# Kernel tuning notes

Measured on AMD Instinct MI355X. Metric: run time of the kernel, lower is better.

Reference implementation:

```python
import jax, jax.numpy as jnp
import numpy as np

B, T, H, STEPS = 8192, 128, 128, 30
BN_EPS = 1e-5


def gru_cell(x, h, w_ih, w_hh, b_ih, b_hh):
    # PyTorch GRU gate math: gates ordered (r, z, n)
    gi = x @ w_ih.T + b_ih            # [B, 3H]
    gh = h @ w_hh.T + b_hh            # [B, 3H]
    ir, iz, inn = jnp.split(gi, 3, axis=-1)
    hr, hz, hn = jnp.split(gh, 3, axis=-1)
    r = jax.nn.sigmoid(ir + hr)
    z = jax.nn.sigmoid(iz + hz)
    n = jnp.tanh(inn + r * hn)
    return (1.0 - z) * n + z * h


def setup_inputs() -> dict:
    key = jax.random.key(0)
    ks = jax.random.split(key, 10)
    s = lambda k, shape: jax.random.normal(k, shape, jnp.float32) * 0.05
    z = lambda *shape: jnp.zeros(shape, jnp.float32)
    return {
        "past": jax.random.normal(ks[0], (B, 6, T), jnp.float32),
        "conv_w": s(ks[1], (H, 6, 3)),
        "conv_b": z(H),
        "bn_gamma": jnp.ones((1,), jnp.float32),
        "bn_beta": z(1),
        "bn_mean": z(1),
        "bn_var": jnp.ones((1,), jnp.float32),
        "enc_wih": s(ks[2], (3 * H, H)),
        "enc_whh": s(ks[3], (3 * H, H)),
        "enc_bih": z(3 * H),
        "enc_bhh": z(3 * H),
        "dec_wih": s(ks[4], (3 * H, H)),
        "dec_whh": s(ks[5], (3 * H, H)),
        "dec_bih": z(3 * H),
        "dec_bhh": z(3 * H),
        "fc1_w": s(ks[6], (256, H)),
        "fc1_b": z(256),
        "fc2_w": s(ks[7], (64, 256)),
        "fc2_b": z(64),
        "fc3_w": s(ks[8], (6, 64)),
        "fc3_b": z(6),
    }


def reference(past, conv_w, conv_b, bn_gamma, bn_beta, bn_mean, bn_var,
              enc_wih, enc_whh, enc_bih, enc_bhh,
              dec_wih, dec_whh, dec_bih, dec_bhh,
              fc1_w, fc1_b, fc2_w, fc2_b, fc3_w, fc3_b):
    b = past.shape[0]
    # Conv1d(6 -> 128, k=3, pad=1) + ReLU
    y = jax.lax.conv_general_dilated(
        past, conv_w, window_strides=(1,), padding=[(1, 1)],
        dimension_numbers=("NCH", "OIH", "NCH"))
    y = jax.nn.relu(y + conv_b[None, :, None])
    # BatchNorm2d(1) in eval mode: single-channel affine normalization over whole tensor
    y = bn_gamma[0] * (y - bn_mean[0]) * jax.lax.rsqrt(bn_var[0] + BN_EPS) + bn_beta[0]
    # encoder GRU over time: [B,128,T] -> [T,B,128]
    xs = jnp.transpose(y, (2, 0, 1))
    h0 = jnp.zeros((b, H), y.dtype)

    def enc_step(h, x):
        return gru_cell(x, h, enc_wih, enc_whh, enc_bih, enc_bhh), None

    state_past, _ = jax.lax.scan(enc_step, h0, xs)  # [B,128]

    def mlp(h):
        a = jax.nn.relu(h @ fc1_w.T + fc1_b)
        a = a @ fc2_w.T + fc2_b   # no activation between fc2 and fc3 (matches Sequential)
        return a @ fc3_w.T + fc3_b

    # decoder input is state_past at step 0, zeros afterwards
    dec_inputs = jnp.concatenate(
        [state_past[None], jnp.zeros((STEPS - 1, b, H), y.dtype)], axis=0)
    present0 = past[:, :, -1]  # [B,6]

    def dec_step(carry, x):
        h, present = carry
        h = gru_cell(x, h, dec_wih, dec_whh, dec_bih, dec_bhh)
        present = present + mlp(h)
        return (h, present), present

    _, preds = jax.lax.scan(dec_step, (jnp.zeros((b, H), y.dtype), present0), dec_inputs)
    # preds: [30,B,6] -> [B,6,30] (matches prediction.permute(0,2,1))
    return jnp.transpose(preds, (1, 2, 0))
```

## Files before the change

### kernel.cpp

```cpp
#include <hip/hip_runtime.h>

#define DI __device__ __forceinline__

typedef __attribute__((ext_vector_type(8))) short short8;
typedef __attribute__((ext_vector_type(4))) float f32x4;

constexpr int THREADS = 512;
constexpr int ROWS    = 32;
constexpr int NBLK    = 8192 / ROWS;
constexpr int PITCH   = 272;
constexpr int PITCH2  = 528;
constexpr int SPITCH  = 256;

constexpr int O_STAGE = 0;
constexpr int O_PATCH = 98304;
constexpr int O_XALL  = 108544;
constexpr int O_H     = 143360;
constexpr int HBUF    = 8704;
constexpr int O_FC3W  = 160768;
constexpr int LDS_TOTAL = 162304;
constexpr int O_A1D   = 98304;
constexpr int O_W32   = 115200;
constexpr int O_B32   = 123648;

DI unsigned cvtpk2(float lo, float hi){
  unsigned r;
  asm("v_cvt_pk_bf16_f32 %0, %1, %2" : "=v"(r) : "v"(lo), "v"(hi));
  return r;
}
DI unsigned short f2bf(float f){ return (unsigned short)cvtpk2(f, f); }
DI float u2f_lo(unsigned u){ union { unsigned u; float f; } v; v.u = u << 16;        return v.f; }
DI float u2f_hi(unsigned u){ union { unsigned u; float f; } v; v.u = u & 0xffff0000u; return v.f; }
DI float sigm(float x){ return __builtin_amdgcn_rcpf(1.f + __expf(-x)); }
DI float tanh_(float x){ return 2.f * __builtin_amdgcn_rcpf(1.f + __expf(-2.f * x)) - 1.f; }
DI f32x4 mfma16(short8 a, short8 b, f32x4 c){
  return __builtin_amdgcn_mfma_f32_16x16x32_bf16(a, b, c, 0, 0, 0);
}
DI uint2 pack4(f32x4 v){
  return make_uint2(cvtpk2(v[0], v[1]), cvtpk2(v[2], v[3]));
}
DI f32x4 unpack4(uint2 u){
  return (f32x4){u2f_lo(u.x), u2f_hi(u.x), u2f_lo(u.y), u2f_hi(u.y)};
}

DI void stage_k128(char* dst, const float* __restrict__ src, int nrows, int tid){
  const int total = nrows * 32;
  for (int i = tid; i < total; i += THREADS){
    float4 v = ((const float4*)src)[i];
    int e = i << 2;
    int n = e >> 7, k = e & 127;
    *(uint2*)(dst + n * SPITCH + k * 2) = make_uint2(cvtpk2(v.x, v.y), cvtpk2(v.z, v.w));
  }
}

__global__ void __launch_bounds__(THREADS, 1)
gru_fused(const float* __restrict__ past,
          const float* __restrict__ conv_w, const float* __restrict__ conv_b,
          const float* __restrict__ bn_gamma, const float* __restrict__ bn_beta,
          const float* __restrict__ bn_mean, const float* __restrict__ bn_var,
          const float* __restrict__ enc_wih, const float* __restrict__ enc_whh,
          const float* __restrict__ enc_bih, const float* __restrict__ enc_bhh,
          const float* __restrict__ dec_wih, const float* __restrict__ dec_whh,
          const float* __restrict__ dec_bih, const float* __restrict__ dec_bhh,
          const float* __restrict__ fc1_w, const float* __restrict__ fc1_b,
          const float* __restrict__ fc2_w, const float* __restrict__ fc2_b,
          const float* __restrict__ fc3_w, const float* __restrict__ fc3_b,
          float* __restrict__ out)
{
  extern __shared__ char smem[];
  const int tid  = threadIdx.x;
  const int lane = tid & 63, w = tid >> 6;
  const int l15  = lane & 15, quad = lane >> 4;
  const int b0   = blockIdx.x * ROWS;
  const int col  = w * 16 + l15;

  const float br_e  = enc_bih[col]       + enc_bhh[col];
  const float bz_e  = enc_bih[128 + col] + enc_bhh[128 + col];
  const float bin_e = enc_bih[256 + col];
  const float bhn_e = enc_bhh[256 + col];
  const float br_d  = dec_bih[col]       + dec_bhh[col];
  const float bz_d  = dec_bih[128 + col] + dec_bhh[128 + col];
  const float bin_d = dec_bih[256 + col];
  const float bhn_d = dec_bhh[256 + col];
  const float cb_t  = conv_b[col];
  const float s_bn  = bn_gamma[0] * rsqrtf(bn_var[0] + 1e-5f);
  const float o_bn  = bn_beta[0] - bn_mean[0] * s_bn;
  const float fb1a  = fc1_b[w * 32 + l15];
  const float fb1b  = fc1_b[w * 32 + 16 + l15];

  for (int i = tid; i < 2*HBUF/4; i += THREADS) ((unsigned*)(smem + O_H))[i] = 0u;

  short8 wf[3][4], wh[3][4];
  stage_k128(smem + O_STAGE, enc_wih, 384, tid);
  __syncthreads();
  #pragma unroll
  for (int g = 0; g < 3; ++g)
    #pragma unroll
    for (int kt = 0; kt < 4; ++kt)
      wf[g][kt] = *(const short8*)(smem + O_STAGE + (g*128 + col)*SPITCH + kt*64 + quad*16);
  __syncthreads();
  stage_k128(smem + O_STAGE, enc_whh, 384, tid);
  __syncthreads();
  #pragma unroll
  for (int g = 0; g < 3; ++g)
    #pragma unroll
    for (int kt = 0; kt < 4; ++kt)
      wh[g][kt] = *(const short8*)(smem + O_STAGE + (g*128 + col)*SPITCH + kt*64 + quad*16);
  __syncthreads();

  for (int i = tid; i < 2560; i += THREADS) ((unsigned*)(smem + O_STAGE))[i] = 0u;
  __syncthreads();
  for (int i = tid; i < 2304; i += THREADS){
    int oc = i / 18, kk = i - oc * 18;
    *(unsigned short*)(smem + O_STAGE + oc*80 + kk*2) = f2bf(conv_w[i]);
  }
  __syncthreads();
  const short8 cwf = *(const short8*)(smem + O_STAGE + col*80 + quad*16);
  __syncthreads();

  for (int i = tid; i < 12672; i += THREADS) ((unsigned*)(smem + O_STAGE))[i] = 0u;
  __syncthreads();
  for (int i4 = tid; i4 < 6144; i4 += THREADS){
    int m = i4 / 192, rem = i4 - m*192, c = rem >> 5, t4 = (rem & 31) << 2;
    float4 v = *(const float4*)(past + (size_t)(b0 + m)*768 + c*128 + t4);
    unsigned short* dst = (unsigned short*)(smem + O_STAGE + ((m*6 + c)*132 + t4 + 1)*2);
    dst[0] = f2bf(v.x); dst[1] = f2bf(v.y); dst[2] = f2bf(v.z); dst[3] = f2bf(v.w);
  }
  for (int i = tid; i < 384; i += THREADS) ((float*)(smem + O_FC3W))[i] = fc3_w[i];
  __syncthreads();

  const int e0 = tid;
  const int m0 = e0 / 18, r0 = e0 - m0*18, c0 = r0 / 3, k0 = r0 - c0*3;
  const int e1 = tid + 512;
  const int m1 = e1 / 18, r1 = e1 - m1*18, c1 = r1 / 3, k1 = r1 - c1*3;

  auto patch_entry = [&](int t0, int m, int r18, int c, int k){
    int base = (m*6 + c)*132 + t0 + k;
    const unsigned* pl = (const unsigned*)(smem + O_STAGE);
    unsigned w0 = pl[base >> 1], w1 = pl[(base >> 1) + 1], w2 = pl[(base >> 1) + 2];
    int sh = (base & 1) * 16;
    unsigned long long lo = (unsigned long long)w0 | ((unsigned long long)w1 << 32);
    unsigned long long hi = (unsigned long long)w1 | ((unsigned long long)w2 << 32);
    unsigned a01 = (unsigned)(lo >> sh);
    unsigned a23 = (unsigned)(hi >> sh);
    char* pb = smem + O_PATCH + m*80 + r18*2;
    *(unsigned short*)(pb)          = (unsigned short)(a01 & 0xffff);
    *(unsigned short*)(pb + 2560)   = (unsigned short)(a01 >> 16);
    *(unsigned short*)(pb + 5120)   = (unsigned short)(a23 & 0xffff);
    *(unsigned short*)(pb + 7680)   = (unsigned short)(a23 >> 16);
  };
  auto patchA1 = [&](int t0){
    patch_entry(t0, m0, r0, c0, k0);
    if (e1 < 576) patch_entry(t0, m1, r1, c1, k1);
  };

  uint2 gi_pk[4][2][3];
  float hreg[8];
  #pragma unroll
  for (int i = 0; i < 8; ++i) hreg[i] = 0.f;

  auto conv_block = [&](){
    #pragma unroll
    for (int mt8 = 0; mt8 < 8; ++mt8){
      short8 pa = *(const short8*)(smem + O_PATCH + (mt8*16 + l15)*80 + quad*16);
      f32x4 cc = (f32x4){0.f,0.f,0.f,0.f};
      cc = mfma16(pa, cwf, cc);
      #pragma unroll
      for (int r = 0; r < 4; ++r){
        int mrow = mt8*16 + quad*4 + r;
        float vx = s_bn * fmaxf(cc[r] + cb_t, 0.f) + o_bn;
        *(unsigned short*)(smem + O_XALL + mrow*PITCH + col*2) = f2bf(vx);
      }
    }
  };
  auto gi_unit = [&](int tc, int mt){
    short8 a[4];
    #pragma unroll
    for (int kt = 0; kt < 4; ++kt)
      a[kt] = *(const short8*)(smem + O_XALL + ((tc*2 + mt)*16 + l15)*PITCH + kt*64 + quad*16);
    f32x4 g0 = (f32x4){0.f,0.f,0.f,0.f}, g1 = g0, g2 = g0;
    #pragma unroll
    for (int kt = 0; kt < 4; ++kt){
      g0 = mfma16(a[kt], wf[0][kt], g0);
      g1 = mfma16(a[kt], wf[1][kt], g1);
      g2 = mfma16(a[kt], wf[2][kt], g2);
    }
    gi_pk[tc][mt][0] = pack4(g0);
    gi_pk[tc][mt][1] = pack4(g1);
    gi_pk[tc][mt][2] = pack4(g2);
  };
  auto step_body = [&](int t, int tc){
    const char* hr = smem + O_H + (t & 1) * HBUF;
    char*       hw = smem + O_H + ((t + 1) & 1) * HBUF;
    f32x4 accr[2], accz[2], accn2[2], gin[2];
    #pragma unroll
    for (int mt = 0; mt < 2; ++mt){
      accr[mt]  = unpack4(gi_pk[tc][mt][0]);
      accz[mt]  = unpack4(gi_pk[tc][mt][1]);
      gin[mt]   = unpack4(gi_pk[tc][mt][2]);
      accn2[mt] = (f32x4){0.f,0.f,0.f,0.f};
    }
    short8 ha[2][4];
    #pragma unroll
    for (int mt = 0; mt < 2; ++mt)
      #pragma unroll
      for (int kt = 0; kt < 4; ++kt)
        ha[mt][kt] = *(const short8*)(hr + (mt*16 + l15)*PITCH + kt*64 + quad*16);
    #pragma unroll
    for (int mt = 0; mt < 2; ++mt)
      #pragma unroll
      for (int kt = 0; kt < 4; ++kt){
        accr[mt]  = mfma16(ha[mt][kt], wh[0][kt], accr[mt]);
        accz[mt]  = mfma16(ha[mt][kt], wh[1][kt], accz[mt]);
        accn2[mt] = mfma16(ha[mt][kt], wh[2][kt], accn2[mt]);
      }
    #pragma unroll
    for (int mt = 0; mt < 2; ++mt)
      #pragma unroll
      for (int r = 0; r < 4; ++r){
        float rg = sigm(accr[mt][r] + br_e);
        float zg = sigm(accz[mt][r] + bz_e);
        float ng = tanh_(gin[mt][r] + bin_e + rg*(accn2[mt][r] + bhn_e));
        hreg[mt*4 + r] = ng + zg*(hreg[mt*4 + r] - ng);
      }
    #pragma unroll
    for (int mt = 0; mt < 2; ++mt)
      #pragma unroll
      for (int r = 0; r < 4; ++r)
        *(unsigned short*)(hw + (mt*16 + quad*4 + r)*PITCH + col*2) = f2bf(hreg[mt*4 + r]);
  };

  patchA1(0);
  __syncthreads();
  conv_block();
  __syncthreads();
  #pragma unroll
  for (int tc = 0; tc < 4; ++tc){ gi_unit(tc, 0); gi_unit(tc, 1); }
  patchA1(4);
  __syncthreads();

  for (int c = 0; c < 32; ++c){
    const int t0 = c * 4;
    const bool prod = (c < 31);
    step_body(t0 + 0, 0);
    if (prod) conv_block();
    __syncthreads();
    step_body(t0 + 1, 1);
    if (prod){ gi_unit(0,0); gi_unit(0,1); gi_unit(1,0); }
    __syncthreads();
    step_body(t0 + 2, 2);
    if (prod){ gi_unit(1,1); gi_unit(2,0); gi_unit(2,1); }
    __syncthreads();
    step_body(t0 + 3, 3);
    if (prod){ gi_unit(3,0); gi_unit(3,1); if (c < 30) patchA1(t0 + 8); }
    __syncthreads();
  }

  stage_k128(smem + O_STAGE, dec_wih, 384, tid);
  __syncthreads();
  #pragma unroll
  for (int g = 0; g < 3; ++g)
    #pragma unroll
    for (int kt = 0; kt < 4; ++kt)
      wf[g][kt] = *(const short8*)(smem + O_STAGE + (g*128 + col)*SPITCH + kt*64 + quad*16);
  f32x4 gi0r[2], gi0z[2], gi0n[2];
  {
    short8 hea[2][4];
    #pragma unroll
    for (int mt = 0; mt < 2; ++mt)
      #pragma unroll
      for (int kt = 0; kt < 4; ++kt)
        hea[mt][kt] = *(const short8*)(smem + O_H + (mt*16 + l15)*PITCH + kt*64 + quad*16);
    #pragma unroll
    for (int mt = 0; mt < 2; ++mt){
      gi0r[mt] = (f32x4){0.f,0.f,0.f,0.f}; gi0z[mt] = gi0r[mt]; gi0n[mt] = gi0r[mt];
      #pragma unroll
      for (int kt = 0; kt < 4; ++kt){
        gi0r[mt] = mfma16(hea[mt][kt], wf[0][kt], gi0r[mt]);
        gi0z[mt] = mfma16(hea[mt][kt], wf[1][kt], gi0z[mt]);
        gi0n[mt] = mfma16(hea[mt][kt], wf[2][kt], gi0n[mt]);
      }
    }
  }
  __syncthreads();
  stage_k128(smem + O_STAGE, dec_whh, 384, tid);
  __syncthreads();
  #pragma unroll
  for (int g = 0; g < 3; ++g)
    #pragma unroll
    for (int kt = 0; kt < 4; ++kt)
      wh[g][kt] = *(const short8*)(smem + O_STAGE + (g*128 + col)*SPITCH + kt*64 + quad*16);
  __syncthreads();
  short8 f1f[2][4];
  stage_k128(smem + O_STAGE, fc1_w, 256, tid);
  __syncthreads();
  #pragma unroll
  for (int j = 0; j < 2; ++j)
    #pragma unroll
    for (int kt = 0; kt < 4; ++kt)
      f1f[j][kt] = *(const short8*)(smem + O_STAGE + (w*32 + j*16 + l15)*SPITCH + kt*64 + quad*16);
  __syncthreads();

  for (int i = tid; i < 2112; i += THREADS) ((unsigned*)(smem + O_W32))[i] = 0u;
  __syncthreads();
  {
    const int kk = tid & 255, wn = (tid >> 8) * 3;
    const float* f3p = (const float*)(smem + O_FC3W);
    float o0 = 0.f, o1 = 0.f, o2 = 0.f;
    for (int j = 0; j < 64; ++j){
      float cv = fc2_w[j*256 + kk];
      o0 += f3p[(wn+0)*64 + j] * cv;
      o1 += f3p[(wn+1)*64 + j] * cv;
      o2 += f3p[(wn+2)*64 + j] * cv;
    }
    *(unsigned short*)(smem + O_W32 + (wn+0)*PITCH2 + kk*2) = f2bf(o0);
    *(unsigned short*)(smem + O_W32 + (wn+1)*PITCH2 + kk*2) = f2bf(o1);
    *(unsigned short*)(smem + O_W32 + (wn+2)*PITCH2 + kk*2) = f2bf(o2);
    if (tid < 6){
      float ob = fc3_b[tid];
      for (int j = 0; j < 64; ++j) ob += f3p[tid*64 + j] * fc2_b[j];
      ((float*)(smem + O_B32))[tid] = ob;
    }
  }
  for (int i = tid; i < HBUF/4; i += THREADS) ((unsigned*)(smem + O_H + HBUF))[i] = 0u;
  #pragma unroll
  for (int i = 0; i < 8; ++i) hreg[i] = 0.f;
  __syncthreads();
  float pres[4] = {0.f, 0.f, 0.f, 0.f};
  float b32v = 0.f;
  if (w < 2 && l15 < 6){
    b32v = ((const float*)(smem + O_B32))[l15];
    #pragma unroll
    for (int r = 0; r < 4; ++r)
      pres[r] = past[(size_t)(b0 + w*16 + quad*4 + r)*768 + l15*128 + 127];
  }

  for (int s = 0; s < 30; ++s){
    const char* hr = smem + O_H + (1 - (s & 1)) * HBUF;
    char*       hw = smem + O_H + (s & 1) * HBUF;
    f32x4 accr[2], accz[2], accn2[2], gin[2];
    #pragma unroll
    for (int mt = 0; mt < 2; ++mt){
      if (s == 0){ accr[mt] = gi0r[mt]; accz[mt] = gi0z[mt]; gin[mt] = gi0n[mt]; }
      else       { accr[mt] = (f32x4){0.f,0.f,0.f,0.f}; accz[mt] = accr[mt]; gin[mt] = accr[mt]; }
      accn2[mt] = (f32x4){0.f,0.f,0.f,0.f};
    }
    {
      short8 ha[2][4];
      #pragma unroll
      for (int mt = 0; mt < 2; ++mt)
        #pragma unroll
        for (int kt = 0; kt < 4; ++kt)
          ha[mt][kt] = *(const short8*)(hr + (mt*16 + l15)*PITCH + kt*64 + quad*16);
      #pragma unroll
      for (int mt = 0; mt < 2; ++mt)
        #pragma unroll
        for (int kt = 0; kt < 4; ++kt){
          accr[mt]  = mfma16(ha[mt][kt], wh[0][kt], accr[mt]);
          accz[mt]  = mfma16(ha[mt][kt], wh[1][kt], accz[mt]);
          accn2[mt] = mfma16(ha[mt][kt], wh[2][kt], accn2[mt]);
        }
    }
    #pragma unroll
    for (int mt = 0; mt < 2; ++mt)
      #pragma unroll
      for (int r = 0; r < 4; ++r){
        float rg = sigm(accr[mt][r] + br_d);
        float zg = sigm(accz[mt][r] + bz_d);
        float ng = tanh_(gin[mt][r] + bin_d + rg*(accn2[mt][r] + bhn_d));
        hreg[mt*4 + r] = ng + zg*(hreg[mt*4 + r] - ng);
      }
    #pragma unroll
    for (int mt = 0; mt < 2; ++mt)
      #pragma unroll
      for (int r = 0; r < 4; ++r)
        *(unsigned short*)(hw + (mt*16 + quad*4 + r)*PITCH + col*2) = f2bf(hreg[mt*4 + r]);
    __syncthreads();

    {
      short8 hf[2][4];
      #pragma unroll
      for (int mt = 0; mt < 2; ++mt)
        #pragma unroll
        for (int kt = 0; kt < 4; ++kt)
          hf[mt][kt] = *(const short8*)(hw + (mt*16 + l15)*PITCH + kt*64 + quad*16);
      f32x4 a1a[2][2];
      #pragma unroll
      for (int mt = 0; mt < 2; ++mt)
        #pragma unroll
        for (int j = 0; j < 2; ++j) a1a[mt][j] = (f32x4){0.f,0.f,0.f,0.f};
      #pragma unroll
      for (int j = 0; j < 2; ++j)
        #pragma unroll
        for (int kt = 0; kt < 4; ++kt){
          a1a[0][j] = mfma16(hf[0][kt], f1f[j][kt], a1a[0][j]);
          a1a[1][j] = mfma16(hf[1][kt], f1f[j][kt], a1a[1][j]);
        }
      #pragma unroll
      for (int mt = 0; mt < 2; ++mt)
        #pragma unroll
        for (int j = 0; j < 2; ++j){
          float bb = j ? fb1b : fb1a;
          #pragma unroll
          for (int r = 0; r < 4; ++r)
            *(unsigned short*)(smem + O_A1D + (mt*16 + quad*4 + r)*PITCH2 +
                               (w*32 + j*16 + l15)*2) = f2bf(fmaxf(a1a[mt][j][r] + bb, 0.f));
        }
    }
    __syncthreads();

    if (w < 2){
      f32x4 acc = (f32x4){0.f,0.f,0.f,0.f};
      #pragma unroll
      for (int kt = 0; kt < 8; ++kt){
        short8 a   = *(const short8*)(smem + O_A1D + (w*16 + l15)*PITCH2 + kt*64 + quad*16);
        short8 bfr = *(const short8*)(smem + O_W32 + l15*PITCH2 + kt*64 + quad*16);
        acc = mfma16(a, bfr, acc);
      }
      if (l15 < 6){
        #pragma unroll
        for (int r = 0; r < 4; ++r){
          pres[r] += acc[r] + b32v;
          out[(size_t)(b0 + w*16 + quad*4 + r)*180 + l15*30 + s] = pres[r];
        }
      }
    }
  }
}

extern "C" void kernel_launch(void* const* d_in, const int* in_sizes, int n_in,
                              void* d_out, int out_size, void* d_ws, size_t ws_size,
                              hipStream_t stream) {
  (void)in_sizes; (void)n_in; (void)out_size; (void)d_ws; (void)ws_size;
  const float* past     = (const float*)d_in[0];
  const float* conv_w   = (const float*)d_in[1];
  const float* conv_b   = (const float*)d_in[2];
  const float* bn_gamma = (const float*)d_in[3];
  const float* bn_beta  = (const float*)d_in[4];
  const float* bn_mean  = (const float*)d_in[5];
  const float* bn_var   = (const float*)d_in[6];
  const float* enc_wih  = (const float*)d_in[7];
  const float* enc_whh  = (const float*)d_in[8];
  const float* enc_bih  = (const float*)d_in[9];
  const float* enc_bhh  = (const float*)d_in[10];
  const float* dec_wih  = (const float*)d_in[11];
  const float* dec_whh  = (const float*)d_in[12];
  const float* dec_bih  = (const float*)d_in[13];
  const float* dec_bhh  = (const float*)d_in[14];
  const float* fc1_w    = (const float*)d_in[15];
  const float* fc1_b    = (const float*)d_in[16];
  const float* fc2_w    = (const float*)d_in[17];
  const float* fc2_b    = (const float*)d_in[18];
  const float* fc3_w    = (const float*)d_in[19];
  const float* fc3_b    = (const float*)d_in[20];

  hipFuncSetAttribute((const void*)gru_fused,
                      hipFuncAttributeMaxDynamicSharedMemorySize, LDS_TOTAL);

  gru_fused<<<NBLK, THREADS, LDS_TOTAL, stream>>>(
      past, conv_w, conv_b, bn_gamma, bn_beta, bn_mean, bn_var,
      enc_wih, enc_whh, enc_bih, enc_bhh,
      dec_wih, dec_whh, dec_bih, dec_bhh,
      fc1_w, fc1_b, fc2_w, fc2_b, fc3_w, fc3_b,
      (float*)d_out);
}
```

Before: 445.4 us.

## Fold log2e into GRU weights and double-buffer decoder FC activations

The log2(e) factors for sigmoid and tanh are folded into the GRU weights and biases when they are staged. This lets the gate math call v_exp_f32 directly with a negated operand, saving a multiply per transcendental. The decoder's first MLP output is double-buffered in LDS, so the fc2/fc3 stage for step s-1 runs after the next step's barrier and one __syncthreads per decoder step is removed. In exchange, the weights are rounded to bf16 after scaling, which slightly changes numerics, and the LDS footprint grows.

```diff
diff --git a/kernel.cpp b/kernel.cpp
--- a/kernel.cpp
+++ b/kernel.cpp
@@ -11,6 +11,9 @@
 constexpr int PITCH   = 272;
 constexpr int PITCH2  = 528;
 constexpr int SPITCH  = 256;
+
+constexpr float L2E  = 1.4426950408889634f;
+constexpr float L2E2 = 2.8853900817779268f;
 
 constexpr int O_STAGE = 0;
 constexpr int O_PATCH = 98304;
@@ -22,6 +25,7 @@
 constexpr int O_A1D   = 98304;
 constexpr int O_W32   = 115200;
 constexpr int O_B32   = 123648;
+constexpr int O_A1D2  = 123680;
 
 DI unsigned cvtpk2(float lo, float hi){
   unsigned r;
@@ -31,8 +35,9 @@
 DI unsigned short f2bf(float f){ return (unsigned short)cvtpk2(f, f); }
 DI float u2f_lo(unsigned u){ union { unsigned u; float f; } v; v.u = u << 16;        return v.f; }
 DI float u2f_hi(unsigned u){ union { unsigned u; float f; } v; v.u = u & 0xffff0000u; return v.f; }
-DI float sigm(float x){ return __builtin_amdgcn_rcpf(1.f + __expf(-x)); }
-DI float tanh_(float x){ return 2.f * __builtin_amdgcn_rcpf(1.f + __expf(-2.f * x)) - 1.f; }
+DI float exp2n(float x){ float r; asm("v_exp_f32 %0, -%1" : "=v"(r) : "v"(x)); return r; }
+DI float sigm2(float s){ return __builtin_amdgcn_rcpf(1.f + exp2n(s)); }
+DI float tanh2(float s){ return 2.f * __builtin_amdgcn_rcpf(1.f + exp2n(s)) - 1.f; }
 DI f32x4 mfma16(short8 a, short8 b, f32x4 c){
   return __builtin_amdgcn_mfma_f32_16x16x32_bf16(a, b, c, 0, 0, 0);
 }
@@ -43,13 +48,16 @@
   return (f32x4){u2f_lo(u.x), u2f_hi(u.x), u2f_lo(u.y), u2f_hi(u.y)};
 }
 
-DI void stage_k128(char* dst, const float* __restrict__ src, int nrows, int tid){
+DI void stage_k128(char* dst, const float* __restrict__ src, int nrows, int tid,
+                   float sA, float sB){
   const int total = nrows * 32;
   for (int i = tid; i < total; i += THREADS){
     float4 v = ((const float4*)src)[i];
     int e = i << 2;
     int n = e >> 7, k = e & 127;
-    *(uint2*)(dst + n * SPITCH + k * 2) = make_uint2(cvtpk2(v.x, v.y), cvtpk2(v.z, v.w));
+    float sc = (n < 256) ? sA : sB;
+    *(uint2*)(dst + n * SPITCH + k * 2) =
+        make_uint2(cvtpk2(v.x * sc, v.y * sc), cvtpk2(v.z * sc, v.w * sc));
   }
 }
 
@@ -74,14 +82,14 @@
   const int b0   = blockIdx.x * ROWS;
   const int col  = w * 16 + l15;
 
-  const float br_e  = enc_bih[col]       + enc_bhh[col];
-  const float bz_e  = enc_bih[128 + col] + enc_bhh[128 + col];
-  const float bin_e = enc_bih[256 + col];
-  const float bhn_e = enc_bhh[256 + col];
-  const float br_d  = dec_bih[col]       + dec_bhh[col];
-  const float bz_d  = dec_bih[128 + col] + dec_bhh[128 + col];
-  const float bin_d = dec_bih[256 + col];
-  const float bhn_d = dec_bhh[256 + col];
+  const float br_e  = (enc_bih[col]       + enc_bhh[col])       * L2E;
+  const float bz_e  = (enc_bih[128 + col] + enc_bhh[128 + col]) * L2E;
+  const float bin_e = enc_bih[256 + col] * L2E2;
+  const float bhn_e = enc_bhh[256 + col] * L2E2;
+  const float br_d  = (dec_bih[col]       + dec_bhh[col])       * L2E;
+  const float bz_d  = (dec_bih[128 + col] + dec_bhh[128 + col]) * L2E;
+  const float bin_d = dec_bih[256 + col] * L2E2;
+  const float bhn_d = dec_bhh[256 + col] * L2E2;
   const float cb_t  = conv_b[col];
   const float s_bn  = bn_gamma[0] * rsqrtf(bn_var[0] + 1e-5f);
   const float o_bn  = bn_beta[0] - bn_mean[0] * s_bn;
@@ -91,7 +99,7 @@
   for (int i = tid; i < 2*HBUF/4; i += THREADS) ((unsigned*)(smem + O_H))[i] = 0u;
 
   short8 wf[3][4], wh[3][4];
-  stage_k128(smem + O_STAGE, enc_wih, 384, tid);
+  stage_k128(smem + O_STAGE, enc_wih, 384, tid, L2E, L2E2);
   __syncthreads();
   #pragma unroll
   for (int g = 0; g < 3; ++g)
@@ -99,7 +107,7 @@
     for (int kt = 0; kt < 4; ++kt)
       wf[g][kt] = *(const short8*)(smem + O_STAGE + (g*128 + col)*SPITCH + kt*64 + quad*16);
   __syncthreads();
-  stage_k128(smem + O_STAGE, enc_whh, 384, tid);
+  stage_k128(smem + O_STAGE, enc_whh, 384, tid, L2E, L2E2);
   __syncthreads();
   #pragma unroll
   for (int g = 0; g < 3; ++g)
@@ -218,9 +226,9 @@
     for (int mt = 0; mt < 2; ++mt)
       #pragma unroll
       for (int r = 0; r < 4; ++r){
-        float rg = sigm(accr[mt][r] + br_e);
-        float zg = sigm(accz[mt][r] + bz_e);
-        float ng = tanh_(gin[mt][r] + bin_e + rg*(accn2[mt][r] + bhn_e));
+        float rg = sigm2(accr[mt][r] + br_e);
+        float zg = sigm2(accz[mt][r] + bz_e);
+        float ng = tanh2(gin[mt][r] + bin_e + rg*(accn2[mt][r] + bhn_e));
         hreg[mt*4 + r] = ng + zg*(hreg[mt*4 + r] - ng);
       }
     #pragma unroll
@@ -256,7 +264,7 @@
     __syncthreads();
   }
 
-  stage_k128(smem + O_STAGE, dec_wih, 384, tid);
+  stage_k128(smem + O_STAGE, dec_wih, 384, tid, L2E, L2E2);
   __syncthreads();
   #pragma unroll
   for (int g = 0; g < 3; ++g)
@@ -283,7 +291,7 @@
     }
   }
   __syncthreads();
-  stage_k128(smem + O_STAGE, dec_whh, 384, tid);
+  stage_k128(smem + O_STAGE, dec_whh, 384, tid, L2E, L2E2);
   __syncthreads();
   #pragma unroll
   for (int g = 0; g < 3; ++g)
@@ -292,7 +300,7 @@
       wh[g][kt] = *(const short8*)(smem + O_STAGE + (g*128 + col)*SPITCH + kt*64 + quad*16);
   __syncthreads();
   short8 f1f[2][4];
-  stage_k128(smem + O_STAGE, fc1_w, 256, tid);
+  stage_k128(smem + O_STAGE, fc1_w, 256, tid, 1.f, 1.f);
   __syncthreads();
   #pragma unroll
   for (int j = 0; j < 2; ++j)
@@ -335,6 +343,24 @@
       pres[r] = past[(size_t)(b0 + w*16 + quad*4 + r)*768 + l15*128 + 127];
   }
 
+  auto fc23 = [&](int sIdx){
+    const char* a1b = smem + ((sIdx & 1) ? O_A1D2 : O_A1D);
+    f32x4 acc = (f32x4){0.f,0.f,0.f,0.f};
+    #pragma unroll
+    for (int kt = 0; kt < 8; ++kt){
+      short8 a   = *(const short8*)(a1b + (w*16 + l15)*PITCH2 + kt*64 + quad*16);
+      short8 bfr = *(const short8*)(smem + O_W32 + l15*PITCH2 + kt*64 + quad*16);
+      acc = mfma16(a, bfr, acc);
+    }
+    if (l15 < 6){
+      #pragma unroll
+      for (int r = 0; r < 4; ++r){
+        pres[r] += acc[r] + b32v;
+        out[(size_t)(b0 + w*16 + quad*4 + r)*180 + l15*30 + sIdx] = pres[r];
+      }
+    }
+  };
+
   for (int s = 0; s < 30; ++s){
     const char* hr = smem + O_H + (1 - (s & 1)) * HBUF;
     char*       hw = smem + O_H + (s & 1) * HBUF;
@@ -365,9 +391,9 @@
     for (int mt = 0; mt < 2; ++mt)
       #pragma unroll
       for (int r = 0; r < 4; ++r){
-        float rg = sigm(accr[mt][r] + br_d);
-        float zg = sigm(accz[mt][r] + bz_d);
-        float ng = tanh_(gin[mt][r] + bin_d + rg*(accn2[mt][r] + bhn_d));
+        float rg = sigm2(accr[mt][r] + br_d);
+        float zg = sigm2(accz[mt][r] + bz_d);
+        float ng = tanh2(gin[mt][r] + bin_d + rg*(accn2[mt][r] + bhn_d));
         hreg[mt*4 + r] = ng + zg*(hreg[mt*4 + r] - ng);
       }
     #pragma unroll
@@ -377,7 +403,10 @@
         *(unsigned short*)(hw + (mt*16 + quad*4 + r)*PITCH + col*2) = f2bf(hreg[mt*4 + r]);
     __syncthreads();
 
+    if (s > 0 && w < 2) fc23(s - 1);
+
     {
+      char* a1w = smem + ((s & 1) ? O_A1D2 : O_A1D);
       short8 hf[2][4];
       #pragma unroll
       for (int mt = 0; mt < 2; ++mt)
@@ -403,29 +432,13 @@
           float bb = j ? fb1b : fb1a;
           #pragma unroll
           for (int r = 0; r < 4; ++r)
-            *(unsigned short*)(smem + O_A1D + (mt*16 + quad*4 + r)*PITCH2 +
+            *(unsigned short*)(a1w + (mt*16 + quad*4 + r)*PITCH2 +
                                (w*32 + j*16 + l15)*2) = f2bf(fmaxf(a1a[mt][j][r] + bb, 0.f));
         }
     }
-    __syncthreads();
-
-    if (w < 2){
-      f32x4 acc = (f32x4){0.f,0.f,0.f,0.f};
-      #pragma unroll
-      for (int kt = 0; kt < 8; ++kt){
-        short8 a   = *(const short8*)(smem + O_A1D + (w*16 + l15)*PITCH2 + kt*64 + quad*16);
-        short8 bfr = *(const short8*)(smem + O_W32 + l15*PITCH2 + kt*64 + quad*16);
-        acc = mfma16(a, bfr, acc);
-      }
-      if (l15 < 6){
-        #pragma unroll
-        for (int r = 0; r < 4; ++r){
-          pres[r] += acc[r] + b32v;
-          out[(size_t)(b0 + w*16 + quad*4 + r)*180 + l15*30 + s] = pres[r];
-        }
-      }
-    }
-  }
+  }
+  __syncthreads();
+  if (w < 2) fc23(29);
 }
 
 extern "C" void kernel_launch(void* const* d_in, const int* in_sizes, int n_in,
```

Result: faster. 425.1 us (median of 2 runs) (-4.6%).
